# Optimization experiments

Hardware: AMD Instinct MI355X
Metric: run time of the kernel (lower is better)

## Reference

```python
import jax, jax.numpy as jnp
import numpy as np

N_NODES = 50000
N_EDGES = 400000
MUL_IN = 32      # input node irreps: 32x0e
MUL_OUT = 64     # target irreps: 64x0e+64x1o+64x2e+64x3o
DENOM = 8.0

# component-normalized real spherical harmonics, l = 1, 2, 3, on unit vectors
_S3, _S5, _S7, _S15, _S42, _S70, _S105 = (np.sqrt(v).astype(np.float32) for v in (3., 5., 7., 15., 42., 70., 105.))

def spherical_harmonics_123(vec):
    # vec: [E, 3]; normalize=True semantics
    r = jnp.linalg.norm(vec, axis=-1, keepdims=True)
    u = vec / jnp.maximum(r, 1e-12)
    x, y, z = u[..., 0], u[..., 1], u[..., 2]
    x2, y2, z2 = x * x, y * y, z * z
    sh1 = jnp.stack([_S3 * x, _S3 * y, _S3 * z], axis=-1)                      # [E, 3]
    sh2 = jnp.stack([
        _S15 * x * y,
        _S15 * y * z,
        0.5 * _S5 * (3.0 * z2 - 1.0),
        _S15 * x * z,
        0.5 * _S15 * (x2 - y2),
    ], axis=-1)                                                                # [E, 5]
    sh3 = jnp.stack([
        0.25 * _S70 * y * (3.0 * x2 - y2),
        _S105 * x * y * z,
        0.25 * _S42 * y * (5.0 * z2 - 1.0),
        0.5 * _S7 * z * (5.0 * z2 - 3.0),
        0.25 * _S42 * x * (5.0 * z2 - 1.0),
        0.5 * _S105 * z * (x2 - y2),
        0.25 * _S70 * x * (x2 - 3.0 * y2),
    ], axis=-1)                                                                # [E, 7]
    return sh1, sh2, sh3


def setup_inputs() -> dict:
    key = jax.random.key(0)
    ks = jax.random.split(key, 9)
    return {
        "positions": jax.random.normal(ks[0], (N_NODES, 3), jnp.float32),
        "node_feats": jax.random.normal(ks[1], (N_NODES, MUL_IN), jnp.float32),
        "W0": jax.random.normal(ks[2], (MUL_IN, MUL_OUT), jnp.float32),
        "W1": jax.random.normal(ks[3], (MUL_IN, MUL_OUT), jnp.float32),
        "W2": jax.random.normal(ks[4], (MUL_IN, MUL_OUT), jnp.float32),
        "W3": jax.random.normal(ks[5], (MUL_IN, MUL_OUT), jnp.float32),
        "Wsc": jax.random.normal(ks[6], (MUL_IN, MUL_OUT), jnp.float32),
        "senders": jax.random.randint(ks[7], (N_EDGES,), 0, N_NODES),
        "receivers": jax.random.randint(ks[8], (N_EDGES,), 0, N_NODES),
    }


def reference(positions, node_feats, W0, W1, W2, W3, Wsc, senders, receivers):
    E = senders.shape[0]
    # ---- update_edge_fn: gather senders, SH of edge vectors, 0e x l tensor product ----
    sf = node_feats[senders]                                      # [E, 32] (32x0e)
    rel = positions[receivers] - positions[senders]               # [E, 3]
    sh1, sh2, sh3 = spherical_harmonics_123(rel)
    # tensor product 32x0e (x) (1o+2e+3o): CG for 0e x l -> l is identity
    tp1 = (sf[:, :, None] * sh1[:, None, :]).reshape(E, -1)       # [E, 32*3]
    tp2 = (sf[:, :, None] * sh2[:, None, :]).reshape(E, -1)       # [E, 32*5]
    tp3 = (sf[:, :, None] * sh3[:, None, :]).reshape(E, -1)       # [E, 32*7]
    messages = jnp.concatenate([sf, tp1, tp2, tp3], axis=-1)      # [E, 512]: 32x0e+32x1o+32x2e+32x3o

    # ---- GraphNetwork aggregation: sum messages at receivers ----
    agg = jax.ops.segment_sum(messages, receivers, num_segments=N_NODES)  # [N, 512]
    nf = agg / DENOM

    # ---- update_node_fn: e3nn Linear per-l (path-normalized by 1/sqrt(fan_in)) ----
    scale = 1.0 / np.sqrt(MUL_IN).astype(np.float32)
    s = nf[:, :MUL_IN]                                            # [N, 32]
    v1 = nf[:, MUL_IN:MUL_IN * 4].reshape(-1, MUL_IN, 3)
    v2 = nf[:, MUL_IN * 4:MUL_IN * 9].reshape(-1, MUL_IN, 5)
    v3 = nf[:, MUL_IN * 9:].reshape(-1, MUL_IN, 7)

    out0 = (s @ W0) * scale                                       # [N, 64]
    out1 = jnp.einsum('nmi,mt->nti', v1, W1) * scale              # [N, 64, 3]
    out2 = jnp.einsum('nmi,mt->nti', v2, W2) * scale              # [N, 64, 5]
    out3 = jnp.einsum('nmi,mt->nti', v3, W3) * scale              # [N, 64, 7]

    # shortcut Linear from 32x0e (force_irreps_out: only the 0e block is nonzero)
    out0 = out0 + (node_feats @ Wsc) * scale

    N = node_feats.shape[0]
    return jnp.concatenate(
        [out0, out1.reshape(N, -1), out2.reshape(N, -1), out3.reshape(N, -1)], axis=-1
    )  # [N, 1024]
```

## Files before the change

### kernel.cpp

```cpp
#include <hip/hip_runtime.h>

#define NN 50000
#define NE 400000
#define SCAN_NB 196

__global__ void k_hist(const int* __restrict__ rcv, int* __restrict__ cnt){
  int e = blockIdx.x*256 + threadIdx.x;
  if (e < NE) atomicAdd(&cnt[rcv[e]], 1);
}

__global__ void k_scanA(const int* __restrict__ cnt, int* __restrict__ bsum){
  __shared__ int sh[256];
  int i = blockIdx.x*256 + threadIdx.x;
  int v = (i < NN) ? cnt[i] : 0;
  sh[threadIdx.x] = v; __syncthreads();
  for (int off=128; off>0; off>>=1){
    if (threadIdx.x < off) sh[threadIdx.x] += sh[threadIdx.x+off];
    __syncthreads();
  }
  if (threadIdx.x==0) bsum[blockIdx.x] = sh[0];
}

__global__ void k_scanB(int* __restrict__ bsum){
  __shared__ int sh[256];
  int t = threadIdx.x;
  int v = (t < SCAN_NB) ? bsum[t] : 0;
  sh[t] = v; __syncthreads();
  for (int off=1; off<256; off<<=1){
    int x = (t>=off)? sh[t-off] : 0;
    __syncthreads();
    sh[t] += x;
    __syncthreads();
  }
  if (t < SCAN_NB) bsum[t] = sh[t] - v;
}

__global__ void k_scanC(const int* __restrict__ cnt, const int* __restrict__ bsum,
                        int* __restrict__ offs, int* __restrict__ cursor){
  __shared__ int sh[256];
  int t = threadIdx.x;
  int i = blockIdx.x*256 + t;
  int v = (i < NN) ? cnt[i] : 0;
  sh[t] = v; __syncthreads();
  for (int off=1; off<256; off<<=1){
    int x = (t>=off)? sh[t-off] : 0;
    __syncthreads();
    sh[t] += x;
    __syncthreads();
  }
  int excl = sh[t] - v + bsum[blockIdx.x];
  if (i < NN){ offs[i] = excl; cursor[i] = excl; }
}

__global__ void k_scatter(const int* __restrict__ rcv, const int* __restrict__ snd,
                          int* __restrict__ cursor, int* __restrict__ csr_snd){
  int e = blockIdx.x*256 + threadIdx.x;
  if (e < NE){
    int p = atomicAdd(&cursor[rcv[e]], 1);
    csr_snd[p] = snd[e];
  }
}

__global__ __launch_bounds__(256) void k_gemm(
    const float* __restrict__ feat,
    const float* __restrict__ W0, const float* __restrict__ W1,
    const float* __restrict__ W2, const float* __restrict__ W3,
    const float* __restrict__ Wsc,
    float4* __restrict__ Ge, float* __restrict__ Gsc)
{
  __shared__ float Wl[5][2048];
  const int tid = threadIdx.x;
  {
    const float* src[5] = {W0,W1,W2,W3,Wsc};
    #pragma unroll
    for (int w=0; w<5; ++w)
      for (int i=tid; i<2048; i+=256)
        Wl[w][i] = src[w][i];
  }
  __syncthreads();
  const int wv = tid>>6, lane = tid&63;
  for (int rep=0; rep<4; ++rep){
    const int n = blockIdx.x*16 + rep*4 + wv;
    const float* fr = feat + (size_t)n*32;
    float a0=0,a1=0,a2=0,a3=0,a4=0;
    #pragma unroll
    for (int m=0; m<32; ++m){
      float f = fr[m];
      a0 += f*Wl[0][m*64+lane];
      a1 += f*Wl[1][m*64+lane];
      a2 += f*Wl[2][m*64+lane];
      a3 += f*Wl[3][m*64+lane];
      a4 += f*Wl[4][m*64+lane];
    }
    Ge[(size_t)n*64 + lane] = make_float4(a0,a1,a2,a3);
    Gsc[(size_t)n*64 + lane] = a4;
  }
}

__global__ __launch_bounds__(256) void k_edge(
    const float* __restrict__ pos, const float4* __restrict__ Ge,
    const float* __restrict__ Gsc, const int* __restrict__ offs,
    const int* __restrict__ cnt, const int* __restrict__ csr_snd,
    float* __restrict__ out)
{
  __shared__ __align__(16) float shb[4][64][16];
  __shared__ int slist[4][64];

  const int tid = threadIdx.x, wv = tid>>6, lane = tid&63;
  const int n = blockIdx.x*4 + wv;
  const float pnx=pos[n*3], pny=pos[n*3+1], pnz=pos[n*3+2];
  const int start = offs[n], deg = cnt[n];
  const int nch = (deg+63)>>6;

  float acc[16];
  #pragma unroll
  for (int k=0;k<16;++k) acc[k]=0.f;

  const float SC3=1.7320508f, SC5=2.236068f, SC7=2.6457513f, SC15=3.8729833f,
              SC42=6.4807407f, SC70=8.3666003f, SC105=10.246951f;

  for (int c=0; c<nch; ++c){
    const int base = c<<6;
    int cn = deg - base; cn = (cn>64)?64:cn;
    if (lane < cn){
      int s = csr_snd[start+base+lane];
      float rx = pnx - pos[s*3];
      float ry = pny - pos[s*3+1];
      float rz = pnz - pos[s*3+2];
      float r = sqrtf(rx*rx+ry*ry+rz*rz);
      float inv = 1.0f/fmaxf(r,1e-12f);
      float x=rx*inv, y=ry*inv, z=rz*inv;
      float x2=x*x, y2=y*y, z2=z*z;
      float s1=SC3*x, s2=SC3*y, s3=SC3*z;
      float s4=SC15*x*y, s5=SC15*y*z, s6=0.5f*SC5*(3.f*z2-1.f), s7=SC15*x*z;
      float s8=0.5f*SC15*(x2-y2);
      float s9 =0.25f*SC70*y*(3.f*x2-y2);
      float s10=SC105*x*y*z;
      float s11=0.25f*SC42*y*(5.f*z2-1.f);
      float s12=0.5f*SC7*z*(5.f*z2-3.f);
      float s13=0.25f*SC42*x*(5.f*z2-1.f);
      float s14=0.5f*SC105*z*(x2-y2);
      float s15=0.25f*SC70*x*(x2-3.f*y2);
      float4* wp = (float4*)&shb[wv][lane][0];
      wp[0] = make_float4(1.0f,s1,s2,s3);
      wp[1] = make_float4(s4,s5,s6,s7);
      wp[2] = make_float4(s8,s9,s10,s11);
      wp[3] = make_float4(s12,s13,s14,s15);
      slist[wv][lane] = s;
    }
    asm volatile("s_waitcnt lgkmcnt(0)" ::: "memory");
    #pragma unroll 4
    for (int it=0; it<cn; ++it){
      int s = __builtin_amdgcn_readfirstlane(slist[wv][it]);
      float4 g = Ge[(size_t)s*64 + lane];
      const float4* rp = (const float4*)&shb[wv][it][0];
      float4 q0=rp[0], q1=rp[1], q2=rp[2], q3=rp[3];
      acc[0] += g.x;
      acc[1] += g.y*q0.y; acc[2] += g.y*q0.z; acc[3] += g.y*q0.w;
      acc[4] += g.z*q1.x; acc[5] += g.z*q1.y; acc[6] += g.z*q1.z;
      acc[7] += g.z*q1.w; acc[8] += g.z*q2.x;
      acc[9] += g.w*q2.y; acc[10]+= g.w*q2.z; acc[11]+= g.w*q2.w;
      acc[12]+= g.w*q3.x; acc[13]+= g.w*q3.y; acc[14]+= g.w*q3.z; acc[15]+= g.w*q3.w;
    }
    asm volatile("" ::: "memory");
  }

  const float S = 0.17677669529663687f;
  const float S8 = S*0.125f;
  float gsc = Gsc[(size_t)n*64 + lane];
  float* o = out + (size_t)n*1024;
  o[lane] = acc[0]*S8 + gsc*S;
  #pragma unroll
  for (int i=0;i<3;++i) o[64  + lane*3 + i] = acc[1+i]*S8;
  #pragma unroll
  for (int i=0;i<5;++i) o[256 + lane*5 + i] = acc[4+i]*S8;
  #pragma unroll
  for (int i=0;i<7;++i) o[576 + lane*7 + i] = acc[9+i]*S8;
}

extern "C" void kernel_launch(void* const* d_in, const int* in_sizes, int n_in,
                              void* d_out, int out_size, void* d_ws, size_t ws_size,
                              hipStream_t stream) {
  const float* pos  = (const float*)d_in[0];
  const float* feat = (const float*)d_in[1];
  const float* W0   = (const float*)d_in[2];
  const float* W1   = (const float*)d_in[3];
  const float* W2   = (const float*)d_in[4];
  const float* W3   = (const float*)d_in[5];
  const float* Wsc  = (const float*)d_in[6];
  const int*  snd   = (const int*)d_in[7];
  const int*  rcv   = (const int*)d_in[8];
  float* out = (float*)d_out;

  int* ws      = (int*)d_ws;
  int* cnt     = ws;
  int* offs    = ws + 50000;
  int* cursor  = ws + 100000;
  int* bsum    = ws + 150000;
  int* csr_snd = ws + 150272;
  float4* Ge   = (float4*)(ws + 550272);
  float*  Gsc  = (float*)(ws + 550272 + 12800000);

  hipMemsetAsync(cnt, 0, NN*sizeof(int), stream);
  k_hist   <<<(NE+255)/256, 256, 0, stream>>>(rcv, cnt);
  k_scanA  <<<SCAN_NB, 256, 0, stream>>>(cnt, bsum);
  k_scanB  <<<1, 256, 0, stream>>>(bsum);
  k_scanC  <<<SCAN_NB, 256, 0, stream>>>(cnt, bsum, offs, cursor);
  k_scatter<<<(NE+255)/256, 256, 0, stream>>>(rcv, snd, cursor, csr_snd);
  k_gemm   <<<3125, 256, 0, stream>>>(feat, W0, W1, W2, W3, Wsc, Ge, Gsc);
  k_edge   <<<12500, 256, 0, stream>>>(pos, Ge, Gsc, offs, cnt, csr_snd, out);
}
```

Baseline: 396.1 us.

## Aggregate raw features times SH per node, then apply weights after aggregation

Reorders the computation so edges accumulate outer products of 32-wide sender features with the 16 spherical-harmonic terms. The per-l weight matrices and shortcut are then applied once per node inside the same kernel, which removes the separate precompute kernel and its large transformed-feature buffer. Per-edge gathers shrink from 64 float4 to 32 floats, and blocks grow to 1024 threads with weights staged in shared memory. In exchange each block does a per-node 32x16x64 contraction, has higher LDS use and lower occupancy, and each block pays for loading all five weight matrices.

```diff
diff --git a/kernel.cpp b/kernel.cpp
--- a/kernel.cpp
+++ b/kernel.cpp
@@ -61,67 +61,45 @@
   }
 }
 
-__global__ __launch_bounds__(256) void k_gemm(
-    const float* __restrict__ feat,
+__global__ __launch_bounds__(1024) void k_edge(
+    const float* __restrict__ pos, const float* __restrict__ feat,
     const float* __restrict__ W0, const float* __restrict__ W1,
     const float* __restrict__ W2, const float* __restrict__ W3,
     const float* __restrict__ Wsc,
-    float4* __restrict__ Ge, float* __restrict__ Gsc)
+    const int* __restrict__ offs, const int* __restrict__ cnt,
+    const int* __restrict__ csr_snd, float* __restrict__ out)
 {
   __shared__ float Wl[5][2048];
+  __shared__ __align__(16) float sm[16][512];
+  __shared__ int slist[16][32];
+
   const int tid = threadIdx.x;
   {
     const float* src[5] = {W0,W1,W2,W3,Wsc};
     #pragma unroll
     for (int w=0; w<5; ++w)
-      for (int i=tid; i<2048; i+=256)
+      for (int i=tid; i<2048; i+=1024)
         Wl[w][i] = src[w][i];
   }
   __syncthreads();
+
   const int wv = tid>>6, lane = tid&63;
-  for (int rep=0; rep<4; ++rep){
-    const int n = blockIdx.x*16 + rep*4 + wv;
-    const float* fr = feat + (size_t)n*32;
-    float a0=0,a1=0,a2=0,a3=0,a4=0;
-    #pragma unroll
-    for (int m=0; m<32; ++m){
-      float f = fr[m];
-      a0 += f*Wl[0][m*64+lane];
-      a1 += f*Wl[1][m*64+lane];
-      a2 += f*Wl[2][m*64+lane];
-      a3 += f*Wl[3][m*64+lane];
-      a4 += f*Wl[4][m*64+lane];
-    }
-    Ge[(size_t)n*64 + lane] = make_float4(a0,a1,a2,a3);
-    Gsc[(size_t)n*64 + lane] = a4;
-  }
-}
-
-__global__ __launch_bounds__(256) void k_edge(
-    const float* __restrict__ pos, const float4* __restrict__ Ge,
-    const float* __restrict__ Gsc, const int* __restrict__ offs,
-    const int* __restrict__ cnt, const int* __restrict__ csr_snd,
-    float* __restrict__ out)
-{
-  __shared__ __align__(16) float shb[4][64][16];
-  __shared__ int slist[4][64];
-
-  const int tid = threadIdx.x, wv = tid>>6, lane = tid&63;
-  const int n = blockIdx.x*4 + wv;
+  const int ml = lane&31, hh = lane>>5;
+  const int n = blockIdx.x*16 + wv;
   const float pnx=pos[n*3], pny=pos[n*3+1], pnz=pos[n*3+2];
   const int start = offs[n], deg = cnt[n];
-  const int nch = (deg+63)>>6;
-
-  float acc[16];
-  #pragma unroll
-  for (int k=0;k<16;++k) acc[k]=0.f;
+  const int nch = (deg+31)>>5;
+
+  float acc[8];
+  #pragma unroll
+  for (int j=0;j<8;++j) acc[j]=0.f;
 
   const float SC3=1.7320508f, SC5=2.236068f, SC7=2.6457513f, SC15=3.8729833f,
               SC42=6.4807407f, SC70=8.3666003f, SC105=10.246951f;
 
   for (int c=0; c<nch; ++c){
-    const int base = c<<6;
-    int cn = deg - base; cn = (cn>64)?64:cn;
+    const int base = c<<5;
+    int cn = deg - base; cn = (cn>32)?32:cn;
     if (lane < cn){
       int s = csr_snd[start+base+lane];
       float rx = pnx - pos[s*3];
@@ -141,7 +119,7 @@
       float s13=0.25f*SC42*x*(5.f*z2-1.f);
       float s14=0.5f*SC105*z*(x2-y2);
       float s15=0.25f*SC70*x*(x2-3.f*y2);
-      float4* wp = (float4*)&shb[wv][lane][0];
+      float4* wp = (float4*)&sm[wv][lane*16];
       wp[0] = make_float4(1.0f,s1,s2,s3);
       wp[1] = make_float4(s4,s5,s6,s7);
       wp[2] = make_float4(s8,s9,s10,s11);
@@ -152,30 +130,59 @@
     #pragma unroll 4
     for (int it=0; it<cn; ++it){
       int s = __builtin_amdgcn_readfirstlane(slist[wv][it]);
-      float4 g = Ge[(size_t)s*64 + lane];
-      const float4* rp = (const float4*)&shb[wv][it][0];
-      float4 q0=rp[0], q1=rp[1], q2=rp[2], q3=rp[3];
-      acc[0] += g.x;
-      acc[1] += g.y*q0.y; acc[2] += g.y*q0.z; acc[3] += g.y*q0.w;
-      acc[4] += g.z*q1.x; acc[5] += g.z*q1.y; acc[6] += g.z*q1.z;
-      acc[7] += g.z*q1.w; acc[8] += g.z*q2.x;
-      acc[9] += g.w*q2.y; acc[10]+= g.w*q2.z; acc[11]+= g.w*q2.w;
-      acc[12]+= g.w*q3.x; acc[13]+= g.w*q3.y; acc[14]+= g.w*q3.z; acc[15]+= g.w*q3.w;
+      float f = feat[(size_t)s*32 + ml];
+      const float4* rp = (const float4*)&sm[wv][it*16 + hh*8];
+      float4 q0=rp[0], q1=rp[1];
+      acc[0]+=f*q0.x; acc[1]+=f*q0.y; acc[2]+=f*q0.z; acc[3]+=f*q0.w;
+      acc[4]+=f*q1.x; acc[5]+=f*q1.y; acc[6]+=f*q1.z; acc[7]+=f*q1.w;
     }
     asm volatile("" ::: "memory");
   }
 
+  {
+    float4* ap = (float4*)&sm[wv][ml*16 + hh*8];
+    ap[0] = make_float4(acc[0],acc[1],acc[2],acc[3]);
+    ap[1] = make_float4(acc[4],acc[5],acc[6],acc[7]);
+  }
+  asm volatile("s_waitcnt lgkmcnt(0)" ::: "memory");
+
+  float oa[16];
+  #pragma unroll
+  for (int k=0;k<16;++k) oa[k]=0.f;
+  float osc = 0.f;
+  const float4* fs4 = (const float4*)(feat + (size_t)n*32);
+
+  #pragma unroll 2
+  for (int g=0; g<8; ++g){
+    float4 fsv = fs4[g];
+    #pragma unroll
+    for (int mm=0; mm<4; ++mm){
+      const int m = g*4+mm;
+      const float fsm = (mm==0)?fsv.x:(mm==1)?fsv.y:(mm==2)?fsv.z:fsv.w;
+      const float4* Ap = (const float4*)&sm[wv][m*16];
+      float4 a0=Ap[0], a1=Ap[1], a2=Ap[2], a3=Ap[3];
+      float w0=Wl[0][m*64+lane], w1=Wl[1][m*64+lane], w2=Wl[2][m*64+lane],
+            w3=Wl[3][m*64+lane], w4=Wl[4][m*64+lane];
+      oa[0] += a0.x*w0;
+      oa[1] += a0.y*w1; oa[2] += a0.z*w1; oa[3] += a0.w*w1;
+      oa[4] += a1.x*w2; oa[5] += a1.y*w2; oa[6] += a1.z*w2;
+      oa[7] += a1.w*w2; oa[8] += a2.x*w2;
+      oa[9] += a2.y*w3; oa[10]+= a2.z*w3; oa[11]+= a2.w*w3;
+      oa[12]+= a3.x*w3; oa[13]+= a3.y*w3; oa[14]+= a3.z*w3; oa[15]+= a3.w*w3;
+      osc += fsm*w4;
+    }
+  }
+
   const float S = 0.17677669529663687f;
   const float S8 = S*0.125f;
-  float gsc = Gsc[(size_t)n*64 + lane];
   float* o = out + (size_t)n*1024;
-  o[lane] = acc[0]*S8 + gsc*S;
-  #pragma unroll
-  for (int i=0;i<3;++i) o[64  + lane*3 + i] = acc[1+i]*S8;
-  #pragma unroll
-  for (int i=0;i<5;++i) o[256 + lane*5 + i] = acc[4+i]*S8;
-  #pragma unroll
-  for (int i=0;i<7;++i) o[576 + lane*7 + i] = acc[9+i]*S8;
+  o[lane] = oa[0]*S8 + osc*S;
+  #pragma unroll
+  for (int i=0;i<3;++i) o[64  + lane*3 + i] = oa[1+i]*S8;
+  #pragma unroll
+  for (int i=0;i<5;++i) o[256 + lane*5 + i] = oa[4+i]*S8;
+  #pragma unroll
+  for (int i=0;i<7;++i) o[576 + lane*7 + i] = oa[9+i]*S8;
 }
 
 extern "C" void kernel_launch(void* const* d_in, const int* in_sizes, int n_in,
@@ -198,8 +205,6 @@
   int* cursor  = ws + 100000;
   int* bsum    = ws + 150000;
   int* csr_snd = ws + 150272;
-  float4* Ge   = (float4*)(ws + 550272);
-  float*  Gsc  = (float*)(ws + 550272 + 12800000);
 
   hipMemsetAsync(cnt, 0, NN*sizeof(int), stream);
   k_hist   <<<(NE+255)/256, 256, 0, stream>>>(rcv, cnt);
@@ -207,6 +212,6 @@
   k_scanB  <<<1, 256, 0, stream>>>(bsum);
   k_scanC  <<<SCAN_NB, 256, 0, stream>>>(cnt, bsum, offs, cursor);
   k_scatter<<<(NE+255)/256, 256, 0, stream>>>(rcv, snd, cursor, csr_snd);
-  k_gemm   <<<3125, 256, 0, stream>>>(feat, W0, W1, W2, W3, Wsc, Ge, Gsc);
-  k_edge   <<<12500, 256, 0, stream>>>(pos, Ge, Gsc, offs, cnt, csr_snd, out);
-}
+  k_edge   <<<3125, 1024, 0, stream>>>(pos, feat, W0, W1, W2, W3, Wsc,
+                                       offs, cnt, csr_snd, out);
+}
```

New measurement: 444.4 us. +12.2%, slower.
